# Kernel tuning notes

Hardware: AMD Instinct MI355X
Metric: run time of the kernel (lower is better)

Reference implementation:

```python
import jax, jax.numpy as jnp
import numpy as np

N = 262144   # memory rows
M = 128      # memory width
N_IN = 128
N_H = 1024
N_OUT = 128
ZDIM = 2 * (M + 5) + 2 * M  # 522


def setup_inputs() -> dict:
    key = jax.random.key(0)
    ks = jax.random.split(key, 12)
    s = 0.02  # param init scale
    return dict(
        x=jax.random.normal(ks[0], (1, N_IN), dtype=jnp.float32),
        h=jax.random.normal(ks[1], (1, N_H), dtype=jnp.float32),
        c=jax.random.normal(ks[2], (1, N_H), dtype=jnp.float32),
        read_weights=jax.random.uniform(ks[3], (1, N), dtype=jnp.float32),
        write_weights=jax.random.uniform(ks[4], (1, N), dtype=jnp.float32),
        memory=jax.random.uniform(ks[5], (N, M), dtype=jnp.float32),
        W_ih=jax.random.normal(ks[6], (4 * N_H, N_IN), dtype=jnp.float32) * s,
        W_hh=jax.random.normal(ks[7], (4 * N_H, N_H), dtype=jnp.float32) * s,
        b_ih=jnp.zeros((4 * N_H,), jnp.float32),
        b_hh=jnp.zeros((4 * N_H,), jnp.float32),
        W_v=jax.random.normal(ks[8], (N_OUT, N_H), dtype=jnp.float32) * s,
        b_v=jnp.zeros((N_OUT,), jnp.float32),
        W_zeta=jax.random.normal(ks[9], (ZDIM, N_H), dtype=jnp.float32) * s,
        b_zeta=jnp.zeros((ZDIM,), jnp.float32),
        W_read=jax.random.normal(ks[10], (N_OUT, M), dtype=jnp.float32) * s,
        b_read=jnp.zeros((N_OUT,), jnp.float32),
    )


def _address(head_params, w_prev, memory):
    # head_params: 1D (>= M+5); w_prev: (N,); memory: (N, M)
    k = head_params[:M]
    g = jax.nn.sigmoid(head_params[M])
    s = jax.nn.softmax(head_params[M + 1:M + 4])
    gamma = 1.0 + jax.nn.softplus(head_params[-1])  # NOTE: [-1] of full slice (faithful quirk)
    mk = memory + 1e-16
    kk = k + 1e-16
    # cosine similarity of each memory row with the key
    sim = (mk @ kk) / jnp.maximum(
        jnp.linalg.norm(mk, axis=1) * jnp.linalg.norm(kk), 1e-8)
    w_c = jax.nn.softmax(sim)                      # content addressing over N
    w_g = g * w_c + (1.0 - g) * w_prev             # interpolation
    # circular shift: w_tild[i] = w_g[i]*s0 + w_g[i+1]*s1 + w_g[i+2]*s2 (mod N)
    w_tild = w_g * s[0] + jnp.roll(w_g, -1) * s[1] + jnp.roll(w_g, -2) * s[2]
    wp = w_tild ** gamma                           # sharpen
    return wp / (jnp.sum(wp) + 1e-16)


def reference(x, h, c, read_weights, write_weights, memory,
              W_ih, W_hh, b_ih, b_hh, W_v, b_v, W_zeta, b_zeta, W_read, b_read):
    # LSTMCell (torch gate order: i, f, g, o)
    gates = x @ W_ih.T + b_ih + h @ W_hh.T + b_hh
    i_g, f_g, g_g, o_g = jnp.split(gates, 4, axis=1)
    c_new = jax.nn.sigmoid(f_g) * c + jax.nn.sigmoid(i_g) * jnp.tanh(g_g)
    h_new = jax.nn.sigmoid(o_g) * jnp.tanh(c_new)
    # NOTE: the original feeds the CELL state into v_fc / zeta_fc (faithful quirk)
    v = c_new @ W_v.T + b_v
    zeta = c_new @ W_zeta.T + b_zeta
    read_params = zeta[0, :M + 5]
    write_params = zeta[0, M + 5:]
    # both heads address the PRE-write memory
    rw = _address(read_params, read_weights[0], memory)   # (N,)
    ww = _address(write_params, write_weights[0], memory)  # (N,)
    erase = write_params[M + 5:M + 5 + M]
    add = write_params[M + 5 + M:]
    mem_new = memory * (1.0 - jnp.outer(ww, erase)) + jnp.outer(ww, add)
    read = rw @ mem_new                                    # (M,)
    y = v + read @ W_read.T + b_read                       # (1, n_out)
    out = jax.nn.log_softmax(y, axis=1)
    return (h_new, c_new, mem_new, out)
```

## Files before the change

### kernel.cpp

```cpp
#include <hip/hip_runtime.h>

#define NTM_N 262144
#define NTM_M 128

#define WS_ZETA    0
#define WS_V       544
#define WS_KKR     672
#define WS_KKW     800
#define WS_ERASE   928
#define WS_ADD     1056
#define WS_SCAL    1184
#define WS_READACC 1216
#define WS_PMAXR   1344
#define WS_PMAXW   2368
#define WS_PSUMR   3392
#define WS_PSUMW   3648
#define WS_PWPR    3904
#define WS_PWPW    4160
#define WS_SIMR    8192
#define WS_SIMW    (8192 + NTM_N)
#define WS_WPR     (8192 + 2*NTM_N)
#define WS_WPW     (8192 + 3*NTM_N)


#define OUT_H 0
#define OUT_C 1024
#define OUT_MEM 2048
#define OUT_Y (2048 + NTM_N * NTM_M)

__device__ __forceinline__ float sigm_(float x) { return 1.f / (1.f + expf(-x)); }
__device__ __forceinline__ float softplus_(float x) {
  return fmaxf(x, 0.f) + log1pf(expf(-fabsf(x)));
}

__global__ __launch_bounds__(256) void lstm_kernel(
    const float* __restrict__ x, const float* __restrict__ h, const float* __restrict__ c,
    const float* __restrict__ W_ih, const float* __restrict__ W_hh,
    const float* __restrict__ b_ih, const float* __restrict__ b_hh,
    float* __restrict__ out) {
  const int wid = (blockIdx.x * blockDim.x + threadIdx.x) >> 6;
  const int lane = threadIdx.x & 63;
  float s0 = 0.f, s1 = 0.f, s2 = 0.f, s3 = 0.f;
  {
    const float* w0 = W_ih + (size_t)(wid)*128;
    const float* w1 = W_ih + (size_t)(1024 + wid) * 128;
    const float* w2 = W_ih + (size_t)(2048 + wid) * 128;
    const float* w3 = W_ih + (size_t)(3072 + wid) * 128;
    for (int t = lane; t < 128; t += 64) {
      float xv = x[t];
      s0 += xv * w0[t]; s1 += xv * w1[t]; s2 += xv * w2[t]; s3 += xv * w3[t];
    }
  }
  {
    const float* w0 = W_hh + (size_t)(wid)*1024;
    const float* w1 = W_hh + (size_t)(1024 + wid) * 1024;
    const float* w2 = W_hh + (size_t)(2048 + wid) * 1024;
    const float* w3 = W_hh + (size_t)(3072 + wid) * 1024;
    for (int t = lane; t < 1024; t += 64) {
      float hv = h[t];
      s0 += hv * w0[t]; s1 += hv * w1[t]; s2 += hv * w2[t]; s3 += hv * w3[t];
    }
  }
#pragma unroll
  for (int off = 32; off; off >>= 1) {
    s0 += __shfl_xor(s0, off); s1 += __shfl_xor(s1, off);
    s2 += __shfl_xor(s2, off); s3 += __shfl_xor(s3, off);
  }
  if (lane == 0) {
    float ig = s0 + b_ih[wid] + b_hh[wid];
    float fg = s1 + b_ih[1024 + wid] + b_hh[1024 + wid];
    float gg = s2 + b_ih[2048 + wid] + b_hh[2048 + wid];
    float og = s3 + b_ih[3072 + wid] + b_hh[3072 + wid];
    float cn = sigm_(fg) * c[wid] + sigm_(ig) * tanhf(gg);
    out[OUT_C + wid] = cn;
    out[OUT_H + wid] = sigm_(og) * tanhf(cn);
  }
}

__global__ __launch_bounds__(256) void zeta_kernel(
    const float* __restrict__ c_new, const float* __restrict__ W_v,
    const float* __restrict__ b_v, const float* __restrict__ W_zeta,
    const float* __restrict__ b_zeta, float* __restrict__ ws) {
  const int wid = (blockIdx.x * blockDim.x + threadIdx.x) >> 6;
  const int lane = threadIdx.x & 63;
  if (wid >= 650) return;
  const float* row;
  float bias;
  int dst;
  if (wid < 522) { row = W_zeta + (size_t)wid * 1024; bias = b_zeta[wid]; dst = WS_ZETA + wid; }
  else { int r = wid - 522; row = W_v + (size_t)r * 1024; bias = b_v[r]; dst = WS_V + r; }
  float p = 0.f;
  for (int t = lane; t < 1024; t += 64) p += c_new[t] * row[t];
#pragma unroll
  for (int off = 32; off; off >>= 1) p += __shfl_xor(p, off);
  if (lane == 0) ws[dst] = p + bias;
}

__global__ __launch_bounds__(128) void params_kernel(float* __restrict__ ws) {
  const int t = threadIdx.x;
  const float* z = ws + WS_ZETA;
  float kr = z[t] + 1e-16f;
  float kw = z[133 + t] + 1e-16f;
  ws[WS_KKR + t] = kr;
  ws[WS_KKW + t] = kw;
  ws[WS_ERASE + t] = z[266 + t];
  ws[WS_ADD + t] = z[394 + t];
  ws[WS_READACC + t] = 0.f;
  __shared__ float red[128];
  red[t] = kr * kr;
  __syncthreads();
  for (int s = 64; s > 0; s >>= 1) { if (t < s) red[t] += red[t + s]; __syncthreads(); }
  if (t == 0) ws[WS_SCAL + 0] = sqrtf(red[0]);
  __syncthreads();
  red[t] = kw * kw;
  __syncthreads();
  for (int s = 64; s > 0; s >>= 1) { if (t < s) red[t] += red[t + s]; __syncthreads(); }
  if (t == 0) {
    ws[WS_SCAL + 1] = sqrtf(red[0]);
    ws[WS_SCAL + 2] = sigm_(z[128]);
    float a0 = z[129], a1 = z[130], a2 = z[131];
    float mx = fmaxf(a0, fmaxf(a1, a2));
    float e0 = expf(a0 - mx), e1 = expf(a1 - mx), e2 = expf(a2 - mx);
    float inv = 1.f / (e0 + e1 + e2);
    ws[WS_SCAL + 4] = e0 * inv; ws[WS_SCAL + 5] = e1 * inv; ws[WS_SCAL + 6] = e2 * inv;
    ws[WS_SCAL + 10] = 1.f + softplus_(z[132]);
    ws[WS_SCAL + 3] = sigm_(z[261]);
    float b0 = z[262], b1 = z[263], b2 = z[264];
    float mb = fmaxf(b0, fmaxf(b1, b2));
    float f0 = expf(b0 - mb), f1 = expf(b1 - mb), f2 = expf(b2 - mb);
    float invb = 1.f / (f0 + f1 + f2);
    ws[WS_SCAL + 7] = f0 * invb; ws[WS_SCAL + 8] = f1 * invb; ws[WS_SCAL + 9] = f2 * invb;
    ws[WS_SCAL + 11] = 1.f + softplus_(z[521]);
  }
}

__global__ __launch_bounds__(256) void sim_kernel(const float* __restrict__ mem,
                                                  float* __restrict__ ws) {
  const int lane = threadIdx.x & 63;
  const int wv = threadIdx.x >> 6;
  const int gw = blockIdx.x * 4 + wv;
  const int row0 = gw * (NTM_N / 4096);
  const float2 kr = *(const float2*)(ws + WS_KKR + 2 * lane);
  const float2 kw = *(const float2*)(ws + WS_KKW + 2 * lane);
  const float nkr = ws[WS_SCAL + 0];
  const float nkw = ws[WS_SCAL + 1];
  float lmr = -3.0e38f, lmw = -3.0e38f;
  for (int i = row0; i < row0 + NTM_N / 4096; ++i) {
    const float2 m2 = *(const float2*)(mem + (size_t)i * 128 + 2 * lane);
    float m0 = m2.x + 1e-16f, m1 = m2.y + 1e-16f;
    float dr = m0 * kr.x + m1 * kr.y;
    float dw = m0 * kw.x + m1 * kw.y;
    float nn = m0 * m0 + m1 * m1;
#pragma unroll
    for (int off = 32; off; off >>= 1) {
      dr += __shfl_xor(dr, off);
      dw += __shfl_xor(dw, off);
      nn += __shfl_xor(nn, off);
    }
    float nrm = sqrtf(nn);
    float sr = dr / fmaxf(nrm * nkr, 1e-8f);
    float sw = dw / fmaxf(nrm * nkw, 1e-8f);
    if (lane == 0) { ws[WS_SIMR + i] = sr; ws[WS_SIMW + i] = sw; }
    lmr = fmaxf(lmr, sr);
    lmw = fmaxf(lmw, sw);
  }
  __shared__ float smr[4], smw[4];
  if (lane == 0) { smr[wv] = lmr; smw[wv] = lmw; }
  __syncthreads();
  if (threadIdx.x == 0) {
    ws[WS_PMAXR + blockIdx.x] = fmaxf(fmaxf(smr[0], smr[1]), fmaxf(smr[2], smr[3]));
    ws[WS_PMAXW + blockIdx.x] = fmaxf(fmaxf(smw[0], smw[1]), fmaxf(smw[2], smw[3]));
  }
}

template <bool IS_MAX>
__global__ __launch_bounds__(256) void reduce2_kernel(float* __restrict__ ws, int srcA, int srcB,
                                                      int n, int dstA, int dstB) {
  const int t = threadIdx.x;
  float a = IS_MAX ? -3.0e38f : 0.f;
  float b = a;
  for (int i = t; i < n; i += 256) {
    float va = ws[srcA + i], vb = ws[srcB + i];
    if (IS_MAX) { a = fmaxf(a, va); b = fmaxf(b, vb); }
    else { a += va; b += vb; }
  }
#pragma unroll
  for (int off = 32; off; off >>= 1) {
    float ax = __shfl_xor(a, off), bx = __shfl_xor(b, off);
    if (IS_MAX) { a = fmaxf(a, ax); b = fmaxf(b, bx); }
    else { a += ax; b += bx; }
  }
  __shared__ float sa[4], sb[4];
  if ((t & 63) == 0) { sa[t >> 6] = a; sb[t >> 6] = b; }
  __syncthreads();
  if (t == 0) {
    float ra = sa[0], rb = sb[0];
    for (int k = 1; k < 4; ++k) {
      if (IS_MAX) { ra = fmaxf(ra, sa[k]); rb = fmaxf(rb, sb[k]); }
      else { ra += sa[k]; rb += sb[k]; }
    }
    ws[dstA] = ra;
    ws[dstB] = rb;
  }
}

__global__ __launch_bounds__(256) void exp_kernel(float* __restrict__ ws) {
  const int tid = threadIdx.x;
  const int idx = (blockIdx.x * 256 + tid) * 4;
  const float mr = ws[WS_SCAL + 12], mw = ws[WS_SCAL + 13];
  float4 sr = *(float4*)(ws + WS_SIMR + idx);
  float4 sw = *(float4*)(ws + WS_SIMW + idx);
  sr.x = expf(sr.x - mr); sr.y = expf(sr.y - mr);
  sr.z = expf(sr.z - mr); sr.w = expf(sr.w - mr);
  sw.x = expf(sw.x - mw); sw.y = expf(sw.y - mw);
  sw.z = expf(sw.z - mw); sw.w = expf(sw.w - mw);
  *(float4*)(ws + WS_SIMR + idx) = sr;
  *(float4*)(ws + WS_SIMW + idx) = sw;
  float pa = (sr.x + sr.y) + (sr.z + sr.w);
  float pb = (sw.x + sw.y) + (sw.z + sw.w);
#pragma unroll
  for (int off = 32; off; off >>= 1) { pa += __shfl_xor(pa, off); pb += __shfl_xor(pb, off); }
  __shared__ float sa[4], sb[4];
  if ((tid & 63) == 0) { sa[tid >> 6] = pa; sb[tid >> 6] = pb; }
  __syncthreads();
  if (tid == 0) {
    ws[WS_PSUMR + blockIdx.x] = (sa[0] + sa[1]) + (sa[2] + sa[3]);
    ws[WS_PSUMW + blockIdx.x] = (sb[0] + sb[1]) + (sb[2] + sb[3]);
  }
}

__global__ __launch_bounds__(256) void convpow_kernel(float* __restrict__ ws,
                                                      const float* __restrict__ rprev,
                                                      const float* __restrict__ wprev) {
  const int tid = threadIdx.x;
  const int base = (blockIdx.x * 256 + tid) * 4;
  const float gr = ws[WS_SCAL + 2], gw_ = ws[WS_SCAL + 3];
  const float s0r = ws[WS_SCAL + 4], s1r = ws[WS_SCAL + 5], s2r = ws[WS_SCAL + 6];
  const float s0w = ws[WS_SCAL + 7], s1w = ws[WS_SCAL + 8], s2w = ws[WS_SCAL + 9];
  const float gar = ws[WS_SCAL + 10], gaw = ws[WS_SCAL + 11];
  const float isr = 1.f / ws[WS_SCAL + 14];
  const float isw = 1.f / ws[WS_SCAL + 15];
  float pa = 0.f, pb = 0.f;
#pragma unroll
  for (int k = 0; k < 4; ++k) {
    int i = base + k;
    int i1 = i + 1; if (i1 >= NTM_N) i1 -= NTM_N;
    int i2 = i + 2; if (i2 >= NTM_N) i2 -= NTM_N;
    {
      float f0 = gr * ws[WS_SIMR + i] * isr + (1.f - gr) * rprev[i];
      float f1 = gr * ws[WS_SIMR + i1] * isr + (1.f - gr) * rprev[i1];
      float f2 = gr * ws[WS_SIMR + i2] * isr + (1.f - gr) * rprev[i2];
      float wt = f0 * s0r + f1 * s1r + f2 * s2r;
      float wp = powf(wt, gar);
      ws[WS_WPR + i] = wp;
      pa += wp;
    }
    {
      float f0 = gw_ * ws[WS_SIMW + i] * isw + (1.f - gw_) * wprev[i];
      float f1 = gw_ * ws[WS_SIMW + i1] * isw + (1.f - gw_) * wprev[i1];
      float f2 = gw_ * ws[WS_SIMW + i2] * isw + (1.f - gw_) * wprev[i2];
      float wt = f0 * s0w + f1 * s1w + f2 * s2w;
      float wp = powf(wt, gaw);
      ws[WS_WPW + i] = wp;
      pb += wp;
    }
  }
#pragma unroll
  for (int off = 32; off; off >>= 1) { pa += __shfl_xor(pa, off); pb += __shfl_xor(pb, off); }
  __shared__ float sa[4], sb[4];
  if ((tid & 63) == 0) { sa[tid >> 6] = pa; sb[tid >> 6] = pb; }
  __syncthreads();
  if (tid == 0) {
    ws[WS_PWPR + blockIdx.x] = (sa[0] + sa[1]) + (sa[2] + sa[3]);
    ws[WS_PWPW + blockIdx.x] = (sb[0] + sb[1]) + (sb[2] + sb[3]);
  }
}

__global__ __launch_bounds__(256) void memupdate_kernel(const float* __restrict__ mem,
                                                        float* __restrict__ out_mem,
                                                        float* __restrict__ ws) {
  const int lane = threadIdx.x & 63;
  const int wv = threadIdx.x >> 6;
  const int gw = blockIdx.x * 4 + wv;
  const int row0 = gw * (NTM_N / 2048);
  const float2 er = *(const float2*)(ws + WS_ERASE + 2 * lane);
  const float2 ad = *(const float2*)(ws + WS_ADD + 2 * lane);
  const float invr = 1.f / (ws[WS_SCAL + 16] + 1e-16f);
  const float invw = 1.f / (ws[WS_SCAL + 17] + 1e-16f);
  float ra = 0.f, rb = 0.f;
  for (int i = row0; i < row0 + NTM_N / 2048; ++i) {
    const float rw = ws[WS_WPR + i] * invr;
    const float wwv = ws[WS_WPW + i] * invw;
    const float2 m2 = *(const float2*)(mem + (size_t)i * 128 + 2 * lane);
    float n0 = m2.x * (1.f - wwv * er.x) + wwv * ad.x;
    float n1 = m2.y * (1.f - wwv * er.y) + wwv * ad.y;
    float2 o2; o2.x = n0; o2.y = n1;
    *(float2*)(out_mem + (size_t)i * 128 + 2 * lane) = o2;
    ra += rw * n0;
    rb += rw * n1;
  }
  __shared__ float sacc[128];
  if (threadIdx.x < 128) sacc[threadIdx.x] = 0.f;
  __syncthreads();
  atomicAdd(&sacc[2 * lane], ra);
  atomicAdd(&sacc[2 * lane + 1], rb);
  __syncthreads();
  if (threadIdx.x < 128) atomicAdd(&ws[WS_READACC + threadIdx.x], sacc[threadIdx.x]);
}

__global__ __launch_bounds__(128) void final_kernel(const float* __restrict__ W_read,
                                                    const float* __restrict__ b_read,
                                                    float* __restrict__ ws,
                                                    float* __restrict__ out_y) {
  const int t = threadIdx.x;
  __shared__ float rd[128];
  rd[t] = ws[WS_READACC + t];
  __syncthreads();
  float y = ws[WS_V + t] + b_read[t];
  const float* wr = W_read + (size_t)t * 128;
  for (int j = 0; j < 128; ++j) y += rd[j] * wr[j];
  __shared__ float red[128];
  red[t] = y;
  __syncthreads();
  for (int s = 64; s > 0; s >>= 1) { if (t < s) red[t] = fmaxf(red[t], red[t + s]); __syncthreads(); }
  float mx = red[0];
  __syncthreads();
  red[t] = expf(y - mx);
  __syncthreads();
  for (int s = 64; s > 0; s >>= 1) { if (t < s) red[t] += red[t + s]; __syncthreads(); }
  float lse = logf(red[0]);
  out_y[t] = y - mx - lse;
}

extern "C" void kernel_launch(void* const* d_in, const int* in_sizes, int n_in,
                              void* d_out, int out_size, void* d_ws, size_t ws_size,
                              hipStream_t stream) {
  const float* x = (const float*)d_in[0];
  const float* h = (const float*)d_in[1];
  const float* c = (const float*)d_in[2];
  const float* rweights = (const float*)d_in[3];
  const float* wweights = (const float*)d_in[4];
  const float* memory = (const float*)d_in[5];
  const float* W_ih = (const float*)d_in[6];
  const float* W_hh = (const float*)d_in[7];
  const float* b_ih = (const float*)d_in[8];
  const float* b_hh = (const float*)d_in[9];
  const float* W_v = (const float*)d_in[10];
  const float* b_v = (const float*)d_in[11];
  const float* W_zeta = (const float*)d_in[12];
  const float* b_zeta = (const float*)d_in[13];
  const float* W_read = (const float*)d_in[14];
  const float* b_read = (const float*)d_in[15];
  float* out = (float*)d_out;
  float* ws = (float*)d_ws;

  lstm_kernel<<<256, 256, 0, stream>>>(x, h, c, W_ih, W_hh, b_ih, b_hh, out);
  zeta_kernel<<<163, 256, 0, stream>>>(out + OUT_C, W_v, b_v, W_zeta, b_zeta, ws);
  params_kernel<<<1, 128, 0, stream>>>(ws);
  sim_kernel<<<1024, 256, 0, stream>>>(memory, ws);
  reduce2_kernel<true><<<1, 256, 0, stream>>>(ws, WS_PMAXR, WS_PMAXW, 1024,
                                              WS_SCAL + 12, WS_SCAL + 13);
  exp_kernel<<<256, 256, 0, stream>>>(ws);
  reduce2_kernel<false><<<1, 256, 0, stream>>>(ws, WS_PSUMR, WS_PSUMW, 256,
                                               WS_SCAL + 14, WS_SCAL + 15);
  convpow_kernel<<<256, 256, 0, stream>>>(ws, rweights, wweights);
  reduce2_kernel<false><<<1, 256, 0, stream>>>(ws, WS_PWPR, WS_PWPW, 256,
                                               WS_SCAL + 16, WS_SCAL + 17);
  memupdate_kernel<<<512, 256, 0, stream>>>(memory, out + OUT_MEM, ws);
  final_kernel<<<1, 128, 0, stream>>>(W_read, b_read, ws, out + OUT_Y);
}
```

Measured before the change: 399.3 us.

## Fuse similarity with exp using fixed max bound, vectorize kernels, spread atomics

Replaces the separate max-reduction and exp passes with one fused kernel. It exponentiates cosine similarity minus 1 directly, relying on cosine similarity being at most 1 so no max pass is needed. The LSTM, zeta, convpow and memupdate kernels are restructured to use float4 loads, with one block per hidden unit in the LSTM and two rows per wavefront. Read-vector atomics are spread across 16 slabs to reduce contention. This removes two launches and a full read-write pass over the similarity arrays. The fixed offset in the softmax could lose precision if similarities are very negative, but the cosine range bounds this.

```diff
diff --git a/kernel.cpp b/kernel.cpp
--- a/kernel.cpp
+++ b/kernel.cpp
@@ -10,13 +10,11 @@
 #define WS_ERASE   928
 #define WS_ADD     1056
 #define WS_SCAL    1184
-#define WS_READACC 1216
-#define WS_PMAXR   1344
-#define WS_PMAXW   2368
-#define WS_PSUMR   3392
-#define WS_PSUMW   3648
-#define WS_PWPR    3904
-#define WS_PWPW    4160
+#define WS_SLAB    1216
+#define WS_PSUMR   3264
+#define WS_PSUMW   5312
+#define WS_PWPR    7360
+#define WS_PWPW    7616
 #define WS_SIMR    8192
 #define WS_SIMW    (8192 + NTM_N)
 #define WS_WPR     (8192 + 2*NTM_N)
@@ -38,42 +36,33 @@
     const float* __restrict__ W_ih, const float* __restrict__ W_hh,
     const float* __restrict__ b_ih, const float* __restrict__ b_hh,
     float* __restrict__ out) {
-  const int wid = (blockIdx.x * blockDim.x + threadIdx.x) >> 6;
-  const int lane = threadIdx.x & 63;
-  float s0 = 0.f, s1 = 0.f, s2 = 0.f, s3 = 0.f;
+  const int j = blockIdx.x;
+  const int wv = threadIdx.x >> 6;
+  const int l = threadIdx.x & 63;
+  const int row = wv * 1024 + j;
+  float s;
   {
-    const float* w0 = W_ih + (size_t)(wid)*128;
-    const float* w1 = W_ih + (size_t)(1024 + wid) * 128;
-    const float* w2 = W_ih + (size_t)(2048 + wid) * 128;
-    const float* w3 = W_ih + (size_t)(3072 + wid) * 128;
-    for (int t = lane; t < 128; t += 64) {
-      float xv = x[t];
-      s0 += xv * w0[t]; s1 += xv * w1[t]; s2 += xv * w2[t]; s3 += xv * w3[t];
-    }
-  }
-  {
-    const float* w0 = W_hh + (size_t)(wid)*1024;
-    const float* w1 = W_hh + (size_t)(1024 + wid) * 1024;
-    const float* w2 = W_hh + (size_t)(2048 + wid) * 1024;
-    const float* w3 = W_hh + (size_t)(3072 + wid) * 1024;
-    for (int t = lane; t < 1024; t += 64) {
-      float hv = h[t];
-      s0 += hv * w0[t]; s1 += hv * w1[t]; s2 += hv * w2[t]; s3 += hv * w3[t];
-    }
-  }
-#pragma unroll
-  for (int off = 32; off; off >>= 1) {
-    s0 += __shfl_xor(s0, off); s1 += __shfl_xor(s1, off);
-    s2 += __shfl_xor(s2, off); s3 += __shfl_xor(s3, off);
-  }
-  if (lane == 0) {
-    float ig = s0 + b_ih[wid] + b_hh[wid];
-    float fg = s1 + b_ih[1024 + wid] + b_hh[1024 + wid];
-    float gg = s2 + b_ih[2048 + wid] + b_hh[2048 + wid];
-    float og = s3 + b_ih[3072 + wid] + b_hh[3072 + wid];
-    float cn = sigm_(fg) * c[wid] + sigm_(ig) * tanhf(gg);
-    out[OUT_C + wid] = cn;
-    out[OUT_H + wid] = sigm_(og) * tanhf(cn);
+    const float2 xv = *(const float2*)(x + 2 * l);
+    const float2 w2 = *(const float2*)(W_ih + (size_t)row * 128 + 2 * l);
+    s = xv.x * w2.x + xv.y * w2.y;
+  }
+  const float* wh = W_hh + (size_t)row * 1024;
+#pragma unroll
+  for (int it = 0; it < 4; ++it) {
+    const int cb = it * 256 + 4 * l;
+    const float4 hv = *(const float4*)(h + cb);
+    const float4 w4 = *(const float4*)(wh + cb);
+    s += hv.x * w4.x + hv.y * w4.y + hv.z * w4.z + hv.w * w4.w;
+  }
+#pragma unroll
+  for (int off = 32; off; off >>= 1) s += __shfl_xor(s, off);
+  __shared__ float gate[4];
+  if (l == 0) gate[wv] = s + b_ih[row] + b_hh[row];
+  __syncthreads();
+  if (threadIdx.x == 0) {
+    const float cn = sigm_(gate[1]) * c[j] + sigm_(gate[0]) * tanhf(gate[2]);
+    out[OUT_C + j] = cn;
+    out[OUT_H + j] = sigm_(gate[3]) * tanhf(cn);
   }
 }
 
@@ -81,31 +70,38 @@
     const float* __restrict__ c_new, const float* __restrict__ W_v,
     const float* __restrict__ b_v, const float* __restrict__ W_zeta,
     const float* __restrict__ b_zeta, float* __restrict__ ws) {
-  const int wid = (blockIdx.x * blockDim.x + threadIdx.x) >> 6;
-  const int lane = threadIdx.x & 63;
+  const int wid = (blockIdx.x * 256 + threadIdx.x) >> 6;
+  const int l = threadIdx.x & 63;
   if (wid >= 650) return;
   const float* row;
   float bias;
   int dst;
   if (wid < 522) { row = W_zeta + (size_t)wid * 1024; bias = b_zeta[wid]; dst = WS_ZETA + wid; }
   else { int r = wid - 522; row = W_v + (size_t)r * 1024; bias = b_v[r]; dst = WS_V + r; }
-  float p = 0.f;
-  for (int t = lane; t < 1024; t += 64) p += c_new[t] * row[t];
-#pragma unroll
-  for (int off = 32; off; off >>= 1) p += __shfl_xor(p, off);
-  if (lane == 0) ws[dst] = p + bias;
+  float s = 0.f;
+#pragma unroll
+  for (int it = 0; it < 4; ++it) {
+    const int cb = it * 256 + 4 * l;
+    const float4 cv = *(const float4*)(c_new + cb);
+    const float4 w4 = *(const float4*)(row + cb);
+    s += cv.x * w4.x + cv.y * w4.y + cv.z * w4.z + cv.w * w4.w;
+  }
+#pragma unroll
+  for (int off = 32; off; off >>= 1) s += __shfl_xor(s, off);
+  if (l == 0) ws[dst] = s + bias;
 }
 
 __global__ __launch_bounds__(128) void params_kernel(float* __restrict__ ws) {
   const int t = threadIdx.x;
   const float* z = ws + WS_ZETA;
-  float kr = z[t] + 1e-16f;
-  float kw = z[133 + t] + 1e-16f;
+  const float kr = z[t] + 1e-16f;
+  const float kw = z[133 + t] + 1e-16f;
   ws[WS_KKR + t] = kr;
   ws[WS_KKW + t] = kw;
   ws[WS_ERASE + t] = z[266 + t];
   ws[WS_ADD + t] = z[394 + t];
-  ws[WS_READACC + t] = 0.f;
+#pragma unroll
+  for (int sl = 0; sl < 16; ++sl) ws[WS_SLAB + sl * 128 + t] = 0.f;
   __shared__ float red[128];
   red[t] = kr * kr;
   __syncthreads();
@@ -134,42 +130,52 @@
   }
 }
 
-__global__ __launch_bounds__(256) void sim_kernel(const float* __restrict__ mem,
-                                                  float* __restrict__ ws) {
-  const int lane = threadIdx.x & 63;
+__global__ __launch_bounds__(256) void simexp_kernel(const float* __restrict__ mem,
+                                                     float* __restrict__ ws) {
+  const int l = threadIdx.x & 63;
   const int wv = threadIdx.x >> 6;
   const int gw = blockIdx.x * 4 + wv;
-  const int row0 = gw * (NTM_N / 4096);
-  const float2 kr = *(const float2*)(ws + WS_KKR + 2 * lane);
-  const float2 kw = *(const float2*)(ws + WS_KKW + 2 * lane);
+  const int half = l >> 5, sl = l & 31;
+  const float4 kr = *(const float4*)(ws + WS_KKR + 4 * sl);
+  const float4 kw = *(const float4*)(ws + WS_KKW + 4 * sl);
   const float nkr = ws[WS_SCAL + 0];
   const float nkw = ws[WS_SCAL + 1];
-  float lmr = -3.0e38f, lmw = -3.0e38f;
-  for (int i = row0; i < row0 + NTM_N / 4096; ++i) {
-    const float2 m2 = *(const float2*)(mem + (size_t)i * 128 + 2 * lane);
-    float m0 = m2.x + 1e-16f, m1 = m2.y + 1e-16f;
-    float dr = m0 * kr.x + m1 * kr.y;
-    float dw = m0 * kw.x + m1 * kw.y;
-    float nn = m0 * m0 + m1 * m1;
-#pragma unroll
-    for (int off = 32; off; off >>= 1) {
+  float lsr = 0.f, lsw = 0.f;
+  const int row0 = gw * 32;
+#pragma unroll 4
+  for (int it = 0; it < 16; ++it) {
+    const int r = row0 + 2 * it + half;
+    const float4 m = *(const float4*)(mem + (size_t)r * 128 + 4 * sl);
+    const float m0 = m.x + 1e-16f, m1 = m.y + 1e-16f;
+    const float m2 = m.z + 1e-16f, m3 = m.w + 1e-16f;
+    float dr = m0 * kr.x + m1 * kr.y + m2 * kr.z + m3 * kr.w;
+    float dw = m0 * kw.x + m1 * kw.y + m2 * kw.z + m3 * kw.w;
+    float nn = m0 * m0 + m1 * m1 + m2 * m2 + m3 * m3;
+#pragma unroll
+    for (int off = 16; off; off >>= 1) {
       dr += __shfl_xor(dr, off);
       dw += __shfl_xor(dw, off);
       nn += __shfl_xor(nn, off);
     }
-    float nrm = sqrtf(nn);
-    float sr = dr / fmaxf(nrm * nkr, 1e-8f);
-    float sw = dw / fmaxf(nrm * nkw, 1e-8f);
-    if (lane == 0) { ws[WS_SIMR + i] = sr; ws[WS_SIMW + i] = sw; }
-    lmr = fmaxf(lmr, sr);
-    lmw = fmaxf(lmw, sw);
-  }
-  __shared__ float smr[4], smw[4];
-  if (lane == 0) { smr[wv] = lmr; smw[wv] = lmw; }
+    if (sl == 0) {
+      const float nrm = sqrtf(nn);
+      const float er = expf(dr / fmaxf(nrm * nkr, 1e-8f) - 1.0f);
+      const float ew = expf(dw / fmaxf(nrm * nkw, 1e-8f) - 1.0f);
+      ws[WS_SIMR + r] = er;
+      ws[WS_SIMW + r] = ew;
+      lsr += er;
+      lsw += ew;
+    }
+  }
+  __shared__ float sa[8], sb[8];
+  if (sl == 0) { sa[wv * 2 + half] = lsr; sb[wv * 2 + half] = lsw; }
   __syncthreads();
   if (threadIdx.x == 0) {
-    ws[WS_PMAXR + blockIdx.x] = fmaxf(fmaxf(smr[0], smr[1]), fmaxf(smr[2], smr[3]));
-    ws[WS_PMAXW + blockIdx.x] = fmaxf(fmaxf(smw[0], smw[1]), fmaxf(smw[2], smw[3]));
+    float ta = 0.f, tb = 0.f;
+#pragma unroll
+    for (int k = 0; k < 8; ++k) { ta += sa[k]; tb += sb[k]; }
+    ws[WS_PSUMR + blockIdx.x] = ta;
+    ws[WS_PSUMW + blockIdx.x] = tb;
   }
 }
 
@@ -180,13 +186,13 @@
   float a = IS_MAX ? -3.0e38f : 0.f;
   float b = a;
   for (int i = t; i < n; i += 256) {
-    float va = ws[srcA + i], vb = ws[srcB + i];
+    const float va = ws[srcA + i], vb = ws[srcB + i];
     if (IS_MAX) { a = fmaxf(a, va); b = fmaxf(b, vb); }
     else { a += va; b += vb; }
   }
 #pragma unroll
   for (int off = 32; off; off >>= 1) {
-    float ax = __shfl_xor(a, off), bx = __shfl_xor(b, off);
+    const float ax = __shfl_xor(a, off), bx = __shfl_xor(b, off);
     if (IS_MAX) { a = fmaxf(a, ax); b = fmaxf(b, bx); }
     else { a += ax; b += bx; }
   }
@@ -201,31 +207,6 @@
     }
     ws[dstA] = ra;
     ws[dstB] = rb;
-  }
-}
-
-__global__ __launch_bounds__(256) void exp_kernel(float* __restrict__ ws) {
-  const int tid = threadIdx.x;
-  const int idx = (blockIdx.x * 256 + tid) * 4;
-  const float mr = ws[WS_SCAL + 12], mw = ws[WS_SCAL + 13];
-  float4 sr = *(float4*)(ws + WS_SIMR + idx);
-  float4 sw = *(float4*)(ws + WS_SIMW + idx);
-  sr.x = expf(sr.x - mr); sr.y = expf(sr.y - mr);
-  sr.z = expf(sr.z - mr); sr.w = expf(sr.w - mr);
-  sw.x = expf(sw.x - mw); sw.y = expf(sw.y - mw);
-  sw.z = expf(sw.z - mw); sw.w = expf(sw.w - mw);
-  *(float4*)(ws + WS_SIMR + idx) = sr;
-  *(float4*)(ws + WS_SIMW + idx) = sw;
-  float pa = (sr.x + sr.y) + (sr.z + sr.w);
-  float pb = (sw.x + sw.y) + (sw.z + sw.w);
-#pragma unroll
-  for (int off = 32; off; off >>= 1) { pa += __shfl_xor(pa, off); pb += __shfl_xor(pb, off); }
-  __shared__ float sa[4], sb[4];
-  if ((tid & 63) == 0) { sa[tid >> 6] = pa; sb[tid >> 6] = pb; }
-  __syncthreads();
-  if (tid == 0) {
-    ws[WS_PSUMR + blockIdx.x] = (sa[0] + sa[1]) + (sa[2] + sa[3]);
-    ws[WS_PSUMW + blockIdx.x] = (sb[0] + sb[1]) + (sb[2] + sb[3]);
   }
 }
 
@@ -240,30 +221,46 @@
   const float gar = ws[WS_SCAL + 10], gaw = ws[WS_SCAL + 11];
   const float isr = 1.f / ws[WS_SCAL + 14];
   const float isw = 1.f / ws[WS_SCAL + 15];
-  float pa = 0.f, pb = 0.f;
-#pragma unroll
-  for (int k = 0; k < 4; ++k) {
-    int i = base + k;
-    int i1 = i + 1; if (i1 >= NTM_N) i1 -= NTM_N;
-    int i2 = i + 2; if (i2 >= NTM_N) i2 -= NTM_N;
-    {
-      float f0 = gr * ws[WS_SIMR + i] * isr + (1.f - gr) * rprev[i];
-      float f1 = gr * ws[WS_SIMR + i1] * isr + (1.f - gr) * rprev[i1];
-      float f2 = gr * ws[WS_SIMR + i2] * isr + (1.f - gr) * rprev[i2];
-      float wt = f0 * s0r + f1 * s1r + f2 * s2r;
-      float wp = powf(wt, gar);
-      ws[WS_WPR + i] = wp;
-      pa += wp;
-    }
-    {
-      float f0 = gw_ * ws[WS_SIMW + i] * isw + (1.f - gw_) * wprev[i];
-      float f1 = gw_ * ws[WS_SIMW + i1] * isw + (1.f - gw_) * wprev[i1];
-      float f2 = gw_ * ws[WS_SIMW + i2] * isw + (1.f - gw_) * wprev[i2];
-      float wt = f0 * s0w + f1 * s1w + f2 * s2w;
-      float wp = powf(wt, gaw);
-      ws[WS_WPW + i] = wp;
-      pb += wp;
-    }
+  int i4 = base + 4; if (i4 >= NTM_N) i4 -= NTM_N;
+  int i5 = base + 5; if (i5 >= NTM_N) i5 -= NTM_N;
+  float pa, pb;
+  {
+    const float4 e0 = *(const float4*)(ws + WS_SIMR + base);
+    const float ea = ws[WS_SIMR + i4], eb = ws[WS_SIMR + i5];
+    const float4 p0 = *(const float4*)(rprev + base);
+    const float pea = rprev[i4], peb = rprev[i5];
+    const float wg0 = gr * e0.x * isr + (1.f - gr) * p0.x;
+    const float wg1 = gr * e0.y * isr + (1.f - gr) * p0.y;
+    const float wg2 = gr * e0.z * isr + (1.f - gr) * p0.z;
+    const float wg3 = gr * e0.w * isr + (1.f - gr) * p0.w;
+    const float wg4 = gr * ea * isr + (1.f - gr) * pea;
+    const float wg5 = gr * eb * isr + (1.f - gr) * peb;
+    float4 wp;
+    wp.x = powf(wg0 * s0r + wg1 * s1r + wg2 * s2r, gar);
+    wp.y = powf(wg1 * s0r + wg2 * s1r + wg3 * s2r, gar);
+    wp.z = powf(wg2 * s0r + wg3 * s1r + wg4 * s2r, gar);
+    wp.w = powf(wg3 * s0r + wg4 * s1r + wg5 * s2r, gar);
+    *(float4*)(ws + WS_WPR + base) = wp;
+    pa = (wp.x + wp.y) + (wp.z + wp.w);
+  }
+  {
+    const float4 e0 = *(const float4*)(ws + WS_SIMW + base);
+    const float ea = ws[WS_SIMW + i4], eb = ws[WS_SIMW + i5];
+    const float4 p0 = *(const float4*)(wprev + base);
+    const float pea = wprev[i4], peb = wprev[i5];
+    const float wg0 = gw_ * e0.x * isw + (1.f - gw_) * p0.x;
+    const float wg1 = gw_ * e0.y * isw + (1.f - gw_) * p0.y;
+    const float wg2 = gw_ * e0.z * isw + (1.f - gw_) * p0.z;
+    const float wg3 = gw_ * e0.w * isw + (1.f - gw_) * p0.w;
+    const float wg4 = gw_ * ea * isw + (1.f - gw_) * pea;
+    const float wg5 = gw_ * eb * isw + (1.f - gw_) * peb;
+    float4 wp;
+    wp.x = powf(wg0 * s0w + wg1 * s1w + wg2 * s2w, gaw);
+    wp.y = powf(wg1 * s0w + wg2 * s1w + wg3 * s2w, gaw);
+    wp.z = powf(wg2 * s0w + wg3 * s1w + wg4 * s2w, gaw);
+    wp.w = powf(wg3 * s0w + wg4 * s1w + wg5 * s2w, gaw);
+    *(float4*)(ws + WS_WPW + base) = wp;
+    pb = (wp.x + wp.y) + (wp.z + wp.w);
   }
 #pragma unroll
   for (int off = 32; off; off >>= 1) { pa += __shfl_xor(pa, off); pb += __shfl_xor(pb, off); }
@@ -279,33 +276,40 @@
 __global__ __launch_bounds__(256) void memupdate_kernel(const float* __restrict__ mem,
                                                         float* __restrict__ out_mem,
                                                         float* __restrict__ ws) {
-  const int lane = threadIdx.x & 63;
+  const int l = threadIdx.x & 63;
   const int wv = threadIdx.x >> 6;
   const int gw = blockIdx.x * 4 + wv;
-  const int row0 = gw * (NTM_N / 2048);
-  const float2 er = *(const float2*)(ws + WS_ERASE + 2 * lane);
-  const float2 ad = *(const float2*)(ws + WS_ADD + 2 * lane);
+  const int half = l >> 5, sl = l & 31;
+  const float4 er4 = *(const float4*)(ws + WS_ERASE + 4 * sl);
+  const float4 ad4 = *(const float4*)(ws + WS_ADD + 4 * sl);
   const float invr = 1.f / (ws[WS_SCAL + 16] + 1e-16f);
   const float invw = 1.f / (ws[WS_SCAL + 17] + 1e-16f);
-  float ra = 0.f, rb = 0.f;
-  for (int i = row0; i < row0 + NTM_N / 2048; ++i) {
-    const float rw = ws[WS_WPR + i] * invr;
-    const float wwv = ws[WS_WPW + i] * invw;
-    const float2 m2 = *(const float2*)(mem + (size_t)i * 128 + 2 * lane);
-    float n0 = m2.x * (1.f - wwv * er.x) + wwv * ad.x;
-    float n1 = m2.y * (1.f - wwv * er.y) + wwv * ad.y;
-    float2 o2; o2.x = n0; o2.y = n1;
-    *(float2*)(out_mem + (size_t)i * 128 + 2 * lane) = o2;
-    ra += rw * n0;
-    rb += rw * n1;
+  float r0 = 0.f, r1 = 0.f, r2 = 0.f, r3 = 0.f;
+  const int row0 = gw * 64;
+#pragma unroll 4
+  for (int it = 0; it < 32; ++it) {
+    const int r = row0 + 2 * it + half;
+    const float rw = ws[WS_WPR + r] * invr;
+    const float wwv = ws[WS_WPW + r] * invw;
+    const float4 m = *(const float4*)(mem + (size_t)r * 128 + 4 * sl);
+    float4 o;
+    o.x = m.x * (1.f - wwv * er4.x) + wwv * ad4.x;
+    o.y = m.y * (1.f - wwv * er4.y) + wwv * ad4.y;
+    o.z = m.z * (1.f - wwv * er4.z) + wwv * ad4.z;
+    o.w = m.w * (1.f - wwv * er4.w) + wwv * ad4.w;
+    *(float4*)(out_mem + (size_t)r * 128 + 4 * sl) = o;
+    r0 += rw * o.x; r1 += rw * o.y; r2 += rw * o.z; r3 += rw * o.w;
   }
   __shared__ float sacc[128];
   if (threadIdx.x < 128) sacc[threadIdx.x] = 0.f;
   __syncthreads();
-  atomicAdd(&sacc[2 * lane], ra);
-  atomicAdd(&sacc[2 * lane + 1], rb);
-  __syncthreads();
-  if (threadIdx.x < 128) atomicAdd(&ws[WS_READACC + threadIdx.x], sacc[threadIdx.x]);
+  atomicAdd(&sacc[4 * sl + 0], r0);
+  atomicAdd(&sacc[4 * sl + 1], r1);
+  atomicAdd(&sacc[4 * sl + 2], r2);
+  atomicAdd(&sacc[4 * sl + 3], r3);
+  __syncthreads();
+  if (threadIdx.x < 128)
+    atomicAdd(&ws[WS_SLAB + (blockIdx.x & 15) * 128 + threadIdx.x], sacc[threadIdx.x]);
 }
 
 __global__ __launch_bounds__(128) void final_kernel(const float* __restrict__ W_read,
@@ -314,7 +318,10 @@
                                                     float* __restrict__ out_y) {
   const int t = threadIdx.x;
   __shared__ float rd[128];
-  rd[t] = ws[WS_READACC + t];
+  float acc = 0.f;
+#pragma unroll
+  for (int s = 0; s < 16; ++s) acc += ws[WS_SLAB + s * 128 + t];
+  rd[t] = acc;
   __syncthreads();
   float y = ws[WS_V + t] + b_read[t];
   const float* wr = W_read + (size_t)t * 128;
@@ -323,12 +330,12 @@
   red[t] = y;
   __syncthreads();
   for (int s = 64; s > 0; s >>= 1) { if (t < s) red[t] = fmaxf(red[t], red[t + s]); __syncthreads(); }
-  float mx = red[0];
+  const float mx = red[0];
   __syncthreads();
   red[t] = expf(y - mx);
   __syncthreads();
   for (int s = 64; s > 0; s >>= 1) { if (t < s) red[t] += red[t + s]; __syncthreads(); }
-  float lse = logf(red[0]);
+  const float lse = logf(red[0]);
   out_y[t] = y - mx - lse;
 }
 
@@ -354,18 +361,15 @@
   float* out = (float*)d_out;
   float* ws = (float*)d_ws;
 
-  lstm_kernel<<<256, 256, 0, stream>>>(x, h, c, W_ih, W_hh, b_ih, b_hh, out);
+  lstm_kernel<<<1024, 256, 0, stream>>>(x, h, c, W_ih, W_hh, b_ih, b_hh, out);
   zeta_kernel<<<163, 256, 0, stream>>>(out + OUT_C, W_v, b_v, W_zeta, b_zeta, ws);
   params_kernel<<<1, 128, 0, stream>>>(ws);
-  sim_kernel<<<1024, 256, 0, stream>>>(memory, ws);
-  reduce2_kernel<true><<<1, 256, 0, stream>>>(ws, WS_PMAXR, WS_PMAXW, 1024,
-                                              WS_SCAL + 12, WS_SCAL + 13);
-  exp_kernel<<<256, 256, 0, stream>>>(ws);
-  reduce2_kernel<false><<<1, 256, 0, stream>>>(ws, WS_PSUMR, WS_PSUMW, 256,
+  simexp_kernel<<<2048, 256, 0, stream>>>(memory, ws);
+  reduce2_kernel<false><<<1, 256, 0, stream>>>(ws, WS_PSUMR, WS_PSUMW, 2048,
                                                WS_SCAL + 14, WS_SCAL + 15);
   convpow_kernel<<<256, 256, 0, stream>>>(ws, rweights, wweights);
   reduce2_kernel<false><<<1, 256, 0, stream>>>(ws, WS_PWPR, WS_PWPW, 256,
                                                WS_SCAL + 16, WS_SCAL + 17);
-  memupdate_kernel<<<512, 256, 0, stream>>>(memory, out + OUT_MEM, ws);
+  memupdate_kernel<<<1024, 256, 0, stream>>>(memory, out + OUT_MEM, ws);
   final_kernel<<<1, 128, 0, stream>>>(W_read, b_read, ws, out + OUT_Y);
 }
```

Result: faster. 330.5 us (-17.2%).
